# Kernel optimization log

Measured on AMD Instinct MI355X. Metric: run time of the kernel, lower is better.

## Reference

```python
import jax, jax.numpy as jnp
import numpy as np


def _pairwise_sqdist(a, b):
    # a: [B,N,3], b: [B,M,3] -> [B,N,M] squared euclidean distances
    d2 = (jnp.sum(a * a, axis=-1)[:, :, None]
          + jnp.sum(b * b, axis=-1)[:, None, :]
          - 2.0 * jnp.einsum('bnd,bmd->bnm', a, b))
    return jnp.maximum(d2, 0.0)


def _knn_idx(a, b, k):
    # indices of k nearest points of b for each point of a: [B,Na,k]
    d2 = jax.lax.stop_gradient(_pairwise_sqdist(a, b))
    _, idx = jax.lax.top_k(-d2, k)
    return idx


def setup_inputs() -> dict:
    key = jax.random.key(0)
    k1, k2 = jax.random.split(key)
    B, N, M = 4, 4096, 100
    xyz = jax.random.normal(k1, (B, N, 6), dtype=jnp.float32)
    skel_xyz = jax.random.normal(k2, (B, M, 3), dtype=jnp.float32)
    return {"xyz": xyz, "num_class": M, "skel_xyz": skel_xyz}


def reference(xyz, num_class, skel_xyz):
    norm = xyz[:, :, 3:6]          # [B,N,3] point normals
    pts = xyz[:, :, :3]            # [B,N,3]
    B, N, _ = pts.shape

    # --- changingrate: per-point normal variation over 10-NN ---
    knn_shape = _knn_idx(pts, pts, 10)                      # [B,N,10]
    n_nb = jax.vmap(lambda n, i: n[i])(norm, knn_shape)     # [B,N,10,3]
    cr = jnp.cross(norm[:, :, None, :], n_nb)               # [B,N,10,3]
    c1 = jnp.linalg.norm(cr, axis=-1)                       # ||n_j x n_k||
    c2 = jnp.linalg.norm(norm[:, :, None, :] * n_nb, axis=-1)  # ||n_j * n_k|| (elementwise)
    changingrate = jnp.sum(jnp.minimum(c1, c2), axis=-1)    # [B,N]

    # --- chamfer-style loss (computed in the original, unused in final_loss) ---
    d2_ps = _pairwise_sqdist(pts, skel_xyz)                 # [B,N,M]
    loss_cd = jnp.sum(jnp.min(d2_ps, axis=2)) / N + jnp.sum(jnp.min(d2_ps, axis=1)) / num_class
    del loss_cd

    # --- voronoi loss: weighted |d1^2 - d2^2| over 2 nearest skeleton pts ---
    _, knn_voroi = jax.lax.top_k(-jax.lax.stop_gradient(d2_ps), 2)   # [B,N,2]
    d12 = jnp.take_along_axis(d2_ps, knn_voroi, axis=2)              # [B,N,2] squared dists
    loss_voronoi = jnp.sum(changingrate * jnp.abs(d12[..., 0] - d12[..., 1]))

    # --- chosen loss: distance to nearest other skeleton point ---
    d2_ss = _pairwise_sqdist(skel_xyz, skel_xyz)            # [B,M,M]
    _, knn_skele = jax.lax.top_k(-jax.lax.stop_gradient(d2_ss), 2)   # [B,M,2]
    diff = skel_xyz - jax.vmap(lambda s, i: s[i])(skel_xyz, knn_skele[..., 1])  # [B,M,3]
    loss_chosen = jnp.sum(jnp.linalg.norm(diff, axis=-1))

    return 1.0 * loss_voronoi - 0.5 * loss_chosen
```

## Files before the change

kernel.cpp:

```cpp
#include <hip/hip_runtime.h>

#define BATCH  4
#define NPTS   4096
#define NSKEL  100
#define KNN    10
#define KL     3
#define QPB    32
#define CPT    64
#define CPAD   65
#define BIG    3.0e38f

__device__ __forceinline__ float med3f(float a, float b, float c) {
#if __has_builtin(__builtin_amdgcn_fmed3f)
    return __builtin_amdgcn_fmed3f(a, b, c);
#else
    float d;
    asm("v_med3_f32 %0, %1, %2, %3" : "=v"(d) : "v"(a), "v"(b), "v"(c));
    return d;
#endif
}

#define CE(a,i,j) do { float _lo = fminf(a[i],a[j]); a[j] = fmaxf(a[i],a[j]); a[i] = _lo; } while (0)
#define SORT10(c) do { \
    CE(c,0,8); CE(c,1,9); \
    CE(c,2,6); CE(c,3,7); CE(c,4,8); CE(c,5,9); \
    CE(c,2,4); CE(c,3,5); CE(c,6,8); CE(c,7,9); CE(c,0,1); \
    CE(c,2,3); CE(c,4,5); CE(c,6,7); CE(c,8,9); } while (0)
#define BM8(c) do { \
    CE(c,0,4); CE(c,1,5); CE(c,2,6); CE(c,3,7); \
    CE(c,0,2); CE(c,1,3); CE(c,4,6); CE(c,5,7); \
    CE(c,0,1); CE(c,2,3); CE(c,4,5); CE(c,6,7); } while (0)

__device__ __forceinline__ void merge_round(float l[KNN], int mask) {
    float c[KNN];
#pragma unroll
    for (int i = 0; i < KNN; ++i) {
        float o = __shfl_xor(l[KNN - 1 - i], mask, 64);
        c[i] = fminf(l[i], o);
    }
    SORT10(c);
#pragma unroll
    for (int i = 0; i < KNN; ++i) l[i] = c[i];
}

#define PIDX(i) ((i) + ((i) >> 6))

__global__ __launch_bounds__(1024) void voronoi_kernel(const float* __restrict__ xyz,
                                                       const float* __restrict__ skel,
                                                       float* __restrict__ out) {
    __shared__ float4 spts[NPTS + 64];
    __shared__ float4 sskl[NSKEL];
    __shared__ float  qlists[QPB][KNN];
    __shared__ float  part[16];

    const int tid = threadIdx.x;
    const int b   = blockIdx.x >> 7;
    const int qb  = (blockIdx.x & 127) * QPB;
    const float* xb = xyz  + (size_t)b * NPTS * 6;
    const float* sb = skel + (size_t)b * NSKEL * 3;

    for (int p2 = tid; p2 < NPTS / 2; p2 += 1024) {
        const float4* row = (const float4*)(xb + p2 * 12);
        float4 A = row[0], Bv = row[1], Cv = row[2];
        int i0 = 2 * p2;
        spts[PIDX(i0)]     = make_float4(A.x, A.y, A.z,
                                         fmaf(A.z, A.z, fmaf(A.y, A.y, A.x * A.x)));
        spts[PIDX(i0 + 1)] = make_float4(Bv.z, Bv.w, Cv.x,
                                         fmaf(Cv.x, Cv.x, fmaf(Bv.w, Bv.w, Bv.z * Bv.z)));
    }
    if (tid < NSKEL) {
        float x = sb[tid*3+0], y = sb[tid*3+1], z = sb[tid*3+2];
        sskl[tid] = make_float4(x, y, z, x*x + y*y + z*z);
    }
    __syncthreads();

    const int split = tid & 31;
    const int group = tid >> 5;
    const int half  = group >> 4;
    const int qpair = group & 15;
    const int q0i   = qb + qpair * 2;
    const float4 Q0 = spts[PIDX(q0i)];
    const float4 Q1 = spts[PIDX(q0i + 1)];
    const float n0x = -2.f*Q0.x, n0y = -2.f*Q0.y, n0z = -2.f*Q0.z;
    const float n1x = -2.f*Q1.x, n1y = -2.f*Q1.y, n1z = -2.f*Q1.z;

    float l0[KL], l1[KL];
#pragma unroll
    for (int k = 0; k < KL; ++k) { l0[k] = BIG; l1[k] = BIG; }

    const int ch = split + (half << 5);
    const unsigned jbc = (unsigned)(ch << 6);
    const unsigned HMASK = 0xFFFFF000u;
    const float4* chunk = spts + ch * CPAD;

#pragma unroll
    for (int g = 0; g < CPT; ++g) {
        float4 cc = chunk[g];
        float s0 = fmaf(n0z, cc.z, fmaf(n0y, cc.y, fmaf(n0x, cc.x, cc.w)));
        float s1 = fmaf(n1z, cc.z, fmaf(n1y, cc.y, fmaf(n1x, cc.x, cc.w)));
        unsigned j = jbc | (unsigned)g;
        float f0 = __uint_as_float((__float_as_uint(s0) & HMASK) | j);
        float f1 = __uint_as_float((__float_as_uint(s1) & HMASK) | j);
        l0[2] = med3f(f0, l0[1], l0[2]);
        l0[1] = med3f(f0, l0[0], l0[1]);
        l0[0] = fminf(f0, l0[0]);
        l1[2] = med3f(f1, l1[1], l1[2]);
        l1[1] = med3f(f1, l1[0], l1[1]);
        l1[0] = fminf(f1, l1[0]);
    }

    float c0[8], c1[8];
    c0[0] = l0[0]; c0[1] = l0[1]; c0[2] = l0[2]; c0[3] = BIG; c0[4] = BIG;
    c0[5] = __shfl_xor(l0[2], 1, 64);
    c0[6] = __shfl_xor(l0[1], 1, 64);
    c0[7] = __shfl_xor(l0[0], 1, 64);
    c1[0] = l1[0]; c1[1] = l1[1]; c1[2] = l1[2]; c1[3] = BIG; c1[4] = BIG;
    c1[5] = __shfl_xor(l1[2], 1, 64);
    c1[6] = __shfl_xor(l1[1], 1, 64);
    c1[7] = __shfl_xor(l1[0], 1, 64);
    BM8(c0);
    BM8(c1);
    const int sel = split & 1;
    float a6[6];
#pragma unroll
    for (int k = 0; k < 6; ++k) a6[k] = sel ? c1[k] : c0[k];

    float ml[KNN];
    {
        float B6[6];
#pragma unroll
        for (int k = 0; k < 6; ++k) B6[k] = __shfl_xor(a6[k], 2, 64);
        ml[0] = a6[0]; ml[1] = a6[1]; ml[2] = a6[2]; ml[3] = a6[3];
        ml[4] = fminf(a6[4], B6[5]);
        ml[5] = fminf(a6[5], B6[4]);
        ml[6] = B6[3]; ml[7] = B6[2]; ml[8] = B6[1]; ml[9] = B6[0];
        SORT10(ml);
    }
    merge_round(ml, 4); merge_round(ml, 8); merge_round(ml, 16);

    if (half == 1 && split < 2) {
#pragma unroll
        for (int k = 0; k < KNN; ++k) qlists[qpair * 2 + split][k] = ml[k];
    }
    __syncthreads();
    if (half == 0 && split < 2) {
        float c[KNN];
#pragma unroll
        for (int i = 0; i < KNN; ++i)
            c[i] = fminf(ml[i], qlists[qpair * 2 + split][KNN - 1 - i]);
#pragma unroll
        for (int k = 0; k < KNN; ++k) qlists[qpair * 2 + split][k] = c[k];
    }
    __syncthreads();

    const int qi = qb + group;
    const float4 Qe = spts[PIDX(qi)];
    const float eqx = -2.f*Qe.x, eqy = -2.f*Qe.y, eqz = -2.f*Qe.z;

    float crk = 0.0f;
    if (split < KNN) {
        int j = (int)(__float_as_uint(qlists[group][split]) & 0xFFFu);
        float nx = xb[qi*6+3], ny = xb[qi*6+4], nz = xb[qi*6+5];
        float mx = xb[j*6+3],  my_ = xb[j*6+4],  mz = xb[j*6+5];
        float cx = ny*mz - nz*my_;
        float cy = nz*mx - nx*mz;
        float cz = nx*my_ - ny*mx;
        float c1 = sqrtf(cx*cx + cy*cy + cz*cz);
        float px = nx*mx, py = ny*my_, pz = nz*mz;
        float c2 = sqrtf(px*px + py*py + pz*pz);
        crk = fminf(c1, c2);
    }
#pragma unroll
    for (int m = 1; m <= 8; m <<= 1) crk += __shfl_xor(crk, m, 64);

    float t0v = BIG, t1v = BIG;
    for (int m = split; m < NSKEL; m += 32) {
        float4 c = sskl[m];
        float s = fmaf(eqz, c.z, fmaf(eqy, c.y, fmaf(eqx, c.x, c.w)));
        t1v = med3f(s, t0v, t1v);
        t0v = fminf(s, t0v);
    }
#pragma unroll
    for (int m = 1; m <= 16; m <<= 1) {
        float o0 = __shfl_xor(t0v, m, 64);
        float o1 = __shfl_xor(t1v, m, 64);
        float nv = fminf(fmaxf(t0v, o0), fminf(t1v, o1));
        t0v = fminf(t0v, o0); t1v = nv;
    }
    float contrib = (split == 0) ? crk * (t1v - t0v) : 0.0f;
    contrib += __shfl_down(contrib, 32);
    if ((tid & 63) == 0) part[tid >> 6] = contrib;
    __syncthreads();
    if (tid == 0) {
        float s = 0.0f;
#pragma unroll
        for (int i = 0; i < 16; ++i) s += part[i];
        atomicAdd(out, s);
    }

    if ((blockIdx.x & 127) == 0) {
        float v = 0.0f;
        if (tid < NSKEL) {
            float4 sq = sskl[tid];
            float b0 = BIG, b1 = BIG; int i0 = 0, i1 = 0;
            for (int jj = 0; jj < NSKEL; ++jj) {
                float4 c = sskl[jj];
                float s = c.w - 2.0f*(sq.x*c.x + sq.y*c.y + sq.z*c.z);
                if (s < b0)      { b1 = b0; i1 = i0; b0 = s; i0 = jj; }
                else if (s < b1) { b1 = s; i1 = jj; }
            }
            float4 c = sskl[i1];
            float dx = sq.x - c.x, dy = sq.y - c.y, dz = sq.z - c.z;
            v = sqrtf(dx*dx + dy*dy + dz*dz);
        }
#pragma unroll
        for (int o = 32; o > 0; o >>= 1) v += __shfl_down(v, o);
        if ((tid & 63) == 0 && tid < 128) atomicAdd(out, -0.5f * v);
    }
}

extern "C" void kernel_launch(void* const* d_in, const int* in_sizes, int n_in,
                              void* d_out, int out_size, void* d_ws, size_t ws_size,
                              hipStream_t stream) {
    const float* xyz  = (const float*)d_in[0];
    const float* skel = (const float*)d_in[2];
    float* out = (float*)d_out;

    hipMemsetAsync(out, 0, sizeof(float), stream);
    voronoi_kernel<<<BATCH * 128, 1024, 0, stream>>>(xyz, skel, out);
}
```

Measured before the change: 39.92 us.

## Double queries per block and drop cross-half KNN merge

Each block now handles 64 queries instead of 32, and each 32-thread group scans all point chunks for its query pair. This removes the split-half merge and one block barrier. The per-point epilogue packs two queries per 32 lanes. The intent is to halve the redundant shared-memory staging of the full point cloud per query. The cost is longer serial scans per thread and half as many blocks.

```diff
diff --git a/kernel.cpp b/kernel.cpp
--- a/kernel.cpp
+++ b/kernel.cpp
@@ -5,9 +5,9 @@
 #define NSKEL  100
 #define KNN    10
 #define KL     3
-#define QPB    32
-#define CPT    64
-#define CPAD   65
+#define QPB    64
+#define CPT    128
+#define CPAD   129
 #define BIG    3.0e38f
 
 __device__ __forceinline__ float med3f(float a, float b, float c) {
@@ -43,19 +43,19 @@
     for (int i = 0; i < KNN; ++i) l[i] = c[i];
 }
 
-#define PIDX(i) ((i) + ((i) >> 6))
+#define PIDX(i) ((i) + ((i) >> 7))
 
 __global__ __launch_bounds__(1024) void voronoi_kernel(const float* __restrict__ xyz,
                                                        const float* __restrict__ skel,
                                                        float* __restrict__ out) {
-    __shared__ float4 spts[NPTS + 64];
+    __shared__ float4 spts[NPTS + 32];
     __shared__ float4 sskl[NSKEL];
     __shared__ float  qlists[QPB][KNN];
     __shared__ float  part[16];
 
     const int tid = threadIdx.x;
-    const int b   = blockIdx.x >> 7;
-    const int qb  = (blockIdx.x & 127) * QPB;
+    const int b   = blockIdx.x >> 6;
+    const int qb  = (blockIdx.x & 63) * QPB;
     const float* xb = xyz  + (size_t)b * NPTS * 6;
     const float* sb = skel + (size_t)b * NSKEL * 3;
 
@@ -76,9 +76,7 @@
 
     const int split = tid & 31;
     const int group = tid >> 5;
-    const int half  = group >> 4;
-    const int qpair = group & 15;
-    const int q0i   = qb + qpair * 2;
+    const int q0i   = qb + group * 2;
     const float4 Q0 = spts[PIDX(q0i)];
     const float4 Q1 = spts[PIDX(q0i + 1)];
     const float n0x = -2.f*Q0.x, n0y = -2.f*Q0.y, n0z = -2.f*Q0.z;
@@ -88,8 +86,8 @@
 #pragma unroll
     for (int k = 0; k < KL; ++k) { l0[k] = BIG; l1[k] = BIG; }
 
-    const int ch = split + (half << 5);
-    const unsigned jbc = (unsigned)(ch << 6);
+    const int ch = split;
+    const unsigned jbc = (unsigned)(ch << 7);
     const unsigned HMASK = 0xFFFFF000u;
     const float4* chunk = spts + ch * CPAD;
 
@@ -138,28 +136,21 @@
     }
     merge_round(ml, 4); merge_round(ml, 8); merge_round(ml, 16);
 
-    if (half == 1 && split < 2) {
-#pragma unroll
-        for (int k = 0; k < KNN; ++k) qlists[qpair * 2 + split][k] = ml[k];
+    if (split < 2) {
+#pragma unroll
+        for (int k = 0; k < KNN; ++k) qlists[group * 2 + split][k] = ml[k];
     }
     __syncthreads();
-    if (half == 0 && split < 2) {
-        float c[KNN];
-#pragma unroll
-        for (int i = 0; i < KNN; ++i)
-            c[i] = fminf(ml[i], qlists[qpair * 2 + split][KNN - 1 - i]);
-#pragma unroll
-        for (int k = 0; k < KNN; ++k) qlists[qpair * 2 + split][k] = c[k];
-    }
-    __syncthreads();
-
-    const int qi = qb + group;
+
+    const int sub  = split >> 4;
+    const int lane = split & 15;
+    const int qi   = qb + group * 2 + sub;
     const float4 Qe = spts[PIDX(qi)];
     const float eqx = -2.f*Qe.x, eqy = -2.f*Qe.y, eqz = -2.f*Qe.z;
 
     float crk = 0.0f;
-    if (split < KNN) {
-        int j = (int)(__float_as_uint(qlists[group][split]) & 0xFFFu);
+    if (lane < KNN) {
+        int j = (int)(__float_as_uint(qlists[group * 2 + sub][lane]) & 0xFFFu);
         float nx = xb[qi*6+3], ny = xb[qi*6+4], nz = xb[qi*6+5];
         float mx = xb[j*6+3],  my_ = xb[j*6+4],  mz = xb[j*6+5];
         float cx = ny*mz - nz*my_;
@@ -174,20 +165,21 @@
     for (int m = 1; m <= 8; m <<= 1) crk += __shfl_xor(crk, m, 64);
 
     float t0v = BIG, t1v = BIG;
-    for (int m = split; m < NSKEL; m += 32) {
+    for (int m = lane; m < NSKEL; m += 16) {
         float4 c = sskl[m];
         float s = fmaf(eqz, c.z, fmaf(eqy, c.y, fmaf(eqx, c.x, c.w)));
         t1v = med3f(s, t0v, t1v);
         t0v = fminf(s, t0v);
     }
 #pragma unroll
-    for (int m = 1; m <= 16; m <<= 1) {
+    for (int m = 1; m <= 8; m <<= 1) {
         float o0 = __shfl_xor(t0v, m, 64);
         float o1 = __shfl_xor(t1v, m, 64);
         float nv = fminf(fmaxf(t0v, o0), fminf(t1v, o1));
         t0v = fminf(t0v, o0); t1v = nv;
     }
-    float contrib = (split == 0) ? crk * (t1v - t0v) : 0.0f;
+    float contrib = (lane == 0) ? crk * (t1v - t0v) : 0.0f;
+    contrib += __shfl_down(contrib, 16);
     contrib += __shfl_down(contrib, 32);
     if ((tid & 63) == 0) part[tid >> 6] = contrib;
     __syncthreads();
@@ -198,7 +190,7 @@
         atomicAdd(out, s);
     }
 
-    if ((blockIdx.x & 127) == 0) {
+    if ((blockIdx.x & 63) == 0) {
         float v = 0.0f;
         if (tid < NSKEL) {
             float4 sq = sskl[tid];
@@ -227,5 +219,5 @@
     float* out = (float*)d_out;
 
     hipMemsetAsync(out, 0, sizeof(float), stream);
-    voronoi_kernel<<<BATCH * 128, 1024, 0, stream>>>(xyz, skel, out);
-}
+    voronoi_kernel<<<BATCH * 64, 1024, 0, stream>>>(xyz, skel, out);
+}
```

Measured after the change: 36.92 us. -7.5%, faster.
